# Optimization experiments

Measured on AMD Instinct MI355X. Metric: run time of the kernel, lower is better.

Reference implementation:

```python
import jax, jax.numpy as jnp
import numpy as np

N_BINS = 25


def setup_inputs() -> dict:
    key = jax.random.key(0)
    k1, k2 = jax.random.split(key)
    logits = jax.random.normal(k1, (500000, 100), dtype=jnp.float32)
    labels = jax.random.randint(k2, (500000,), 0, 100, dtype=jnp.int64)
    return {"logits": logits, "labels": labels}


def reference(logits, labels):
    # softmax confidences + predictions
    probs = jax.nn.softmax(logits, axis=1)
    confidences = jnp.max(probs, axis=1)              # [N]
    predictions = jnp.argmax(probs, axis=1)           # [N]
    accuracies = (predictions == labels).astype(jnp.float32)

    # Equal-width bins over (0,1]: bin i covers (i/n_bins, (i+1)/n_bins].
    # conf > lower AND conf <= upper  <=>  bin = ceil(conf*n_bins)-1 (conf>0 always for softmax).
    bins = jnp.clip(jnp.ceil(confidences * N_BINS).astype(jnp.int32) - 1, 0, N_BINS - 1)

    counts = jax.ops.segment_sum(jnp.ones_like(confidences), bins, num_segments=N_BINS)
    sum_conf = jax.ops.segment_sum(confidences, bins, num_segments=N_BINS)
    sum_acc = jax.ops.segment_sum(accuracies, bins, num_segments=N_BINS)

    n = jnp.float32(confidences.shape[0])
    prop_in_bin = counts / n
    safe_counts = jnp.maximum(counts, 1.0)
    avg_conf = sum_conf / safe_counts
    avg_acc = sum_acc / safe_counts

    ece = jnp.sum(jnp.where(counts > 0, jnp.abs(avg_conf - avg_acc) * prop_in_bin, 0.0))
    return ece
```

## Files before the change

### kernel.cpp

```cpp
#include <hip/hip_runtime.h>
#include <cfloat>

#define NBINS 25

__launch_bounds__(256, 8)
__global__ void ece_pass1(const float* __restrict__ logits,
                          const int* __restrict__ labels,
                          float* __restrict__ ws, int n) {
    __shared__ float s_cnt[NBINS], s_conf[NBINS], s_acc[NBINS];
    if (threadIdx.x < NBINS) {
        s_cnt[threadIdx.x]  = 0.f;
        s_conf[threadIdx.x] = 0.f;
        s_acc[threadIdx.x]  = 0.f;
    }
    __syncthreads();

    const int lane = threadIdx.x & 63;
    const int j    = lane & 3;
    const int g    = lane >> 2;
    const int wid  = (int)((blockIdx.x * blockDim.x + threadIdx.x) >> 6);
    const int nw   = (int)((gridDim.x * blockDim.x) >> 6);

    for (int base = wid * 16; base < n; base += nw * 16) {
        const int row = base + g;
        const bool rowok = row < n;
        const float4* rp = reinterpret_cast<const float4*>(logits) + (size_t)row * 25;

        float4 v[7];
#pragma unroll
        for (int k = 0; k < 6; ++k) {
            v[k] = rowok ? rp[j + 4 * k]
                         : make_float4(-FLT_MAX, -FLT_MAX, -FLT_MAX, -FLT_MAX);
        }
        v[6] = (rowok && j == 0) ? rp[24]
                                 : make_float4(-FLT_MAX, -FLT_MAX, -FLT_MAX, -FLT_MAX);

        float m = -FLT_MAX; int mi = 0;
#pragma unroll
        for (int k = 0; k < 7; ++k) {
            const int q = j + 4 * k;
            const int idx = 4 * q;
            if (v[k].x > m) { m = v[k].x; mi = idx; }
            if (v[k].y > m) { m = v[k].y; mi = idx + 1; }
            if (v[k].z > m) { m = v[k].z; mi = idx + 2; }
            if (v[k].w > m) { m = v[k].w; mi = idx + 3; }
        }
#pragma unroll
        for (int off = 1; off <= 2; off <<= 1) {
            float om = __shfl_xor(m, off);
            int   oi = __shfl_xor(mi, off);
            if (om > m || (om == m && oi < mi)) { m = om; mi = oi; }
        }

        float s = 0.f;
#pragma unroll
        for (int k = 0; k < 7; ++k) {
            const int q = j + 4 * k;
            if (q < 25) {
                s += __expf(v[k].x - m) + __expf(v[k].y - m) +
                     __expf(v[k].z - m) + __expf(v[k].w - m);
            }
        }
#pragma unroll
        for (int off = 1; off <= 2; off <<= 1) s += __shfl_xor(s, off);

        if (rowok && j == 0) {
            float conf = 1.0f / s;
            int bin = (int)ceilf(conf * (float)NBINS) - 1;
            bin = min(max(bin, 0), NBINS - 1);
            float acc = (mi == labels[row]) ? 1.f : 0.f;
            atomicAdd(&s_cnt[bin], 1.f);
            atomicAdd(&s_conf[bin], conf);
            atomicAdd(&s_acc[bin], acc);
        }
    }
    __syncthreads();
    if (threadIdx.x < NBINS) {
        atomicAdd(&ws[threadIdx.x],             s_cnt[threadIdx.x]);
        atomicAdd(&ws[NBINS + threadIdx.x],     s_conf[threadIdx.x]);
        atomicAdd(&ws[2 * NBINS + threadIdx.x], s_acc[threadIdx.x]);
    }
}

__global__ void ece_final(const float* __restrict__ ws, float* __restrict__ out, float n) {
    int t = threadIdx.x;
    float term = 0.f;
    if (t < NBINS) {
        float cnt = ws[t];
        float sc  = ws[NBINS + t];
        float sa  = ws[2 * NBINS + t];
        if (cnt > 0.f) {
            float inv = 1.f / cnt;
            term = fabsf(sc * inv - sa * inv) * (cnt / n);
        }
    }
#pragma unroll
    for (int off = 32; off; off >>= 1) term += __shfl_xor(term, off);
    if (t == 0) out[0] = term;
}

extern "C" void kernel_launch(void* const* d_in, const int* in_sizes, int n_in,
                              void* d_out, int out_size, void* d_ws, size_t ws_size,
                              hipStream_t stream) {
    const float* logits = (const float*)d_in[0];
    const int*   labels = (const int*)d_in[1];
    float* ws  = (float*)d_ws;
    float* out = (float*)d_out;
    const int n = in_sizes[1];

    hipMemsetAsync(ws, 0, 3 * NBINS * sizeof(float), stream);

    const int block = 256;
    const int grid  = 2048;
    ece_pass1<<<grid, block, 0, stream>>>(logits, labels, ws, n);
    ece_final<<<1, 64, 0, stream>>>(ws, out, (float)n);
}
```

Before: 312.2 us.

## Stage logit tiles in LDS with coalesced loads; replace global atomics with partials

Each block now copies a 128-row chunk of logits into shared memory using fully coalesced float4 loads, then computes per-row max/argmax/softmax sum from LDS instead of strided per-row global reads. The global atomic accumulation and memset are replaced by per-block partial histograms written to workspace and reduced by a 1024-thread final kernel. This adds 51KB of LDS per block, limiting occupancy to about three blocks per CU, and adds barriers between load and compute with no overlap.

Result: slower. 334.7 us (+7.2%).

```diff
diff --git a/kernel.cpp b/kernel.cpp
--- a/kernel.cpp
+++ b/kernel.cpp
@@ -2,101 +2,122 @@
 #include <cfloat>
 
 #define NBINS 25
+#define RPB   128
+#define THREADS 256
+#define GRID1 1024
 
-__launch_bounds__(256, 8)
+__launch_bounds__(THREADS, 3)
 __global__ void ece_pass1(const float* __restrict__ logits,
                           const int* __restrict__ labels,
-                          float* __restrict__ ws, int n) {
+                          float* __restrict__ part, int n) {
+    __shared__ float tile[RPB * 100];
     __shared__ float s_cnt[NBINS], s_conf[NBINS], s_acc[NBINS];
-    if (threadIdx.x < NBINS) {
-        s_cnt[threadIdx.x]  = 0.f;
-        s_conf[threadIdx.x] = 0.f;
-        s_acc[threadIdx.x]  = 0.f;
-    }
-    __syncthreads();
+    const int t = threadIdx.x;
+    if (t < NBINS) { s_cnt[t] = 0.f; s_conf[t] = 0.f; s_acc[t] = 0.f; }
 
-    const int lane = threadIdx.x & 63;
-    const int j    = lane & 3;
-    const int g    = lane >> 2;
-    const int wid  = (int)((blockIdx.x * blockDim.x + threadIdx.x) >> 6);
-    const int nw   = (int)((gridDim.x * blockDim.x) >> 6);
+    const int j = t & 3;
+    const int g = t >> 2;
 
-    for (int base = wid * 16; base < n; base += nw * 16) {
-        const int row = base + g;
-        const bool rowok = row < n;
-        const float4* rp = reinterpret_cast<const float4*>(logits) + (size_t)row * 25;
+    for (int c = blockIdx.x; c * RPB < n; c += GRID1) {
+        const int base = c * RPB;
+        const int rows = min(RPB, n - base);
+        const int nf4  = rows * 25;
 
-        float4 v[7];
+        const float4* src = reinterpret_cast<const float4*>(logits) + (size_t)base * 25;
+        float4* dst = reinterpret_cast<float4*>(tile);
 #pragma unroll
-        for (int k = 0; k < 6; ++k) {
-            v[k] = rowok ? rp[j + 4 * k]
-                         : make_float4(-FLT_MAX, -FLT_MAX, -FLT_MAX, -FLT_MAX);
+        for (int k = 0; k < 13; ++k) {
+            const int idx = t + k * THREADS;
+            if (idx < nf4) dst[idx] = src[idx];
         }
-        v[6] = (rowok && j == 0) ? rp[24]
-                                 : make_float4(-FLT_MAX, -FLT_MAX, -FLT_MAX, -FLT_MAX);
+        __syncthreads();
 
-        float m = -FLT_MAX; int mi = 0;
 #pragma unroll
-        for (int k = 0; k < 7; ++k) {
-            const int q = j + 4 * k;
-            const int idx = 4 * q;
-            if (v[k].x > m) { m = v[k].x; mi = idx; }
-            if (v[k].y > m) { m = v[k].y; mi = idx + 1; }
-            if (v[k].z > m) { m = v[k].z; mi = idx + 2; }
-            if (v[k].w > m) { m = v[k].w; mi = idx + 3; }
-        }
+        for (int rr = 0; rr < RPB; rr += 64) {
+            const int r = rr + g;
+            const float* rowp = tile + r * 100;
+            float4 v[6];
 #pragma unroll
-        for (int off = 1; off <= 2; off <<= 1) {
-            float om = __shfl_xor(m, off);
-            int   oi = __shfl_xor(mi, off);
-            if (om > m || (om == m && oi < mi)) { m = om; mi = oi; }
-        }
+            for (int k = 0; k < 6; ++k)
+                v[k] = *reinterpret_cast<const float4*>(rowp + (j + 4 * k) * 4);
+            const float x24 = rowp[96 + j];
 
-        float s = 0.f;
+            float m = v[0].x; int mi = 4 * j;
+            if (v[0].y > m) { m = v[0].y; mi = 4 * j + 1; }
+            if (v[0].z > m) { m = v[0].z; mi = 4 * j + 2; }
+            if (v[0].w > m) { m = v[0].w; mi = 4 * j + 3; }
 #pragma unroll
-        for (int k = 0; k < 7; ++k) {
-            const int q = j + 4 * k;
-            if (q < 25) {
+            for (int k = 1; k < 6; ++k) {
+                const int idx = 4 * (j + 4 * k);
+                if (v[k].x > m) { m = v[k].x; mi = idx; }
+                if (v[k].y > m) { m = v[k].y; mi = idx + 1; }
+                if (v[k].z > m) { m = v[k].z; mi = idx + 2; }
+                if (v[k].w > m) { m = v[k].w; mi = idx + 3; }
+            }
+            if (x24 > m) { m = x24; mi = 96 + j; }
+#pragma unroll
+            for (int off = 1; off <= 2; off <<= 1) {
+                const float om = __shfl_xor(m, off);
+                const int   oi = __shfl_xor(mi, off);
+                if (om > m || (om == m && oi < mi)) { m = om; mi = oi; }
+            }
+            float s = __expf(x24 - m);
+#pragma unroll
+            for (int k = 0; k < 6; ++k) {
                 s += __expf(v[k].x - m) + __expf(v[k].y - m) +
                      __expf(v[k].z - m) + __expf(v[k].w - m);
             }
+#pragma unroll
+            for (int off = 1; off <= 2; off <<= 1) s += __shfl_xor(s, off);
+
+            if (j == 0 && r < rows) {
+                const float conf = 1.0f / s;
+                int bin = (int)ceilf(conf * (float)NBINS) - 1;
+                bin = min(max(bin, 0), NBINS - 1);
+                const float acc = (mi == labels[base + r]) ? 1.f : 0.f;
+                atomicAdd(&s_cnt[bin], 1.f);
+                atomicAdd(&s_conf[bin], conf);
+                atomicAdd(&s_acc[bin], acc);
+            }
         }
-#pragma unroll
-        for (int off = 1; off <= 2; off <<= 1) s += __shfl_xor(s, off);
+        __syncthreads();
+    }
 
-        if (rowok && j == 0) {
-            float conf = 1.0f / s;
-            int bin = (int)ceilf(conf * (float)NBINS) - 1;
-            bin = min(max(bin, 0), NBINS - 1);
-            float acc = (mi == labels[row]) ? 1.f : 0.f;
-            atomicAdd(&s_cnt[bin], 1.f);
-            atomicAdd(&s_conf[bin], conf);
-            atomicAdd(&s_acc[bin], acc);
-        }
-    }
-    __syncthreads();
-    if (threadIdx.x < NBINS) {
-        atomicAdd(&ws[threadIdx.x],             s_cnt[threadIdx.x]);
-        atomicAdd(&ws[NBINS + threadIdx.x],     s_conf[threadIdx.x]);
-        atomicAdd(&ws[2 * NBINS + threadIdx.x], s_acc[threadIdx.x]);
+    if (t < NBINS) {
+        part[t * GRID1 + blockIdx.x]               = s_cnt[t];
+        part[(NBINS + t) * GRID1 + blockIdx.x]     = s_conf[t];
+        part[(2 * NBINS + t) * GRID1 + blockIdx.x] = s_acc[t];
     }
 }
 
-__global__ void ece_final(const float* __restrict__ ws, float* __restrict__ out, float n) {
-    int t = threadIdx.x;
-    float term = 0.f;
-    if (t < NBINS) {
-        float cnt = ws[t];
-        float sc  = ws[NBINS + t];
-        float sa  = ws[2 * NBINS + t];
-        if (cnt > 0.f) {
-            float inv = 1.f / cnt;
-            term = fabsf(sc * inv - sa * inv) * (cnt / n);
+__global__ void ece_final(const float* __restrict__ part, float* __restrict__ out, float n) {
+    __shared__ float sacc[3 * NBINS];
+    const int t = threadIdx.x;
+    const int wave = t >> 6, lane = t & 63;
+    for (int slot = wave; slot < 3 * NBINS; slot += 16) {
+        const float* p = part + slot * GRID1;
+        float s = 0.f;
+        for (int k = lane; k < GRID1; k += 64) s += p[k];
+#pragma unroll
+        for (int off = 32; off; off >>= 1) s += __shfl_xor(s, off);
+        if (lane == 0) sacc[slot] = s;
+    }
+    __syncthreads();
+    if (t < 64) {
+        float term = 0.f;
+        if (t < NBINS) {
+            const float cnt = sacc[t];
+            const float sc  = sacc[NBINS + t];
+            const float sa  = sacc[2 * NBINS + t];
+            if (cnt > 0.f) {
+                const float inv = 1.f / cnt;
+                term = fabsf(sc * inv - sa * inv) * (cnt / n);
+            }
         }
+#pragma unroll
+        for (int off = 32; off; off >>= 1) term += __shfl_xor(term, off);
+        if (t == 0) out[0] = term;
     }
-#pragma unroll
-    for (int off = 32; off; off >>= 1) term += __shfl_xor(term, off);
-    if (t == 0) out[0] = term;
 }
 
 extern "C" void kernel_launch(void* const* d_in, const int* in_sizes, int n_in,
@@ -104,14 +125,10 @@
                               hipStream_t stream) {
     const float* logits = (const float*)d_in[0];
     const int*   labels = (const int*)d_in[1];
-    float* ws  = (float*)d_ws;
-    float* out = (float*)d_out;
+    float* part = (float*)d_ws;
+    float* out  = (float*)d_out;
     const int n = in_sizes[1];
 
-    hipMemsetAsync(ws, 0, 3 * NBINS * sizeof(float), stream);
-
-    const int block = 256;
-    const int grid  = 2048;
-    ece_pass1<<<grid, block, 0, stream>>>(logits, labels, ws, n);
-    ece_final<<<1, 64, 0, stream>>>(ws, out, (float)n);
+    ece_pass1<<<GRID1, THREADS, 0, stream>>>(logits, labels, part, n);
+    ece_final<<<1, 1024, 0, stream>>>(part, out, (float)n);
 }
```
